# Performance work log

Measured on AMD Instinct MI355X. Metric: run time of the kernel, lower is better.

The kernel has to match this reference:

```python
import jax, jax.numpy as jnp
import numpy as np
from jax.scipy.linalg import solve_triangular

OMEGA0 = 30.0  # standard SIREN first-layer frequency


def setup_inputs() -> dict:
    key = jax.random.key(0)
    ks = jax.random.split(key, 12)
    B, NC, NT, XD, H, R = 64, 1024, 1024, 1, 512, 512
    x_context = jax.random.normal(ks[0], (B, NC, XD), jnp.float32)
    y_context = jax.random.normal(ks[1], (B, NC, 1), jnp.float32)
    x_target = jax.random.normal(ks[2], (B, NT, XD), jnp.float32)
    # SIREN MLP params (hidden_dims=[512,512,512], repr_dim=512)
    def lin(k, fi, fo, first=False):
        bound = 1.0 / fi if first else np.sqrt(6.0 / fi) / OMEGA0
        kW, kb = jax.random.split(k)
        W = jax.random.uniform(kW, (fi, fo), jnp.float32, -bound, bound)
        b = jax.random.uniform(kb, (fo,), jnp.float32, -bound, bound)
        return W, b
    W0, b0 = lin(ks[3], XD, H, first=True)
    W1, b1 = lin(ks[4], H, H)
    W2, b2 = lin(ks[5], H, H)
    Wr, br = lin(ks[6], H, R)
    log_noise_var = jnp.asarray(np.log(0.01), jnp.float32)
    return {"x_context": x_context, "y_context": y_context, "x_target": x_target,
            "W0": W0, "b0": b0, "W1": W1, "b1": b1, "W2": W2, "b2": b2,
            "Wr": Wr, "br": br, "log_noise_var": log_noise_var}


def _mlp(x, W0, b0, W1, b1, W2, b2, Wr, br):
    # SIREN: sine activations, omega_0 on first layer, linear head
    h = jnp.sin(OMEGA0 * (x @ W0 + b0))
    h = jnp.sin(h @ W1 + b1)
    h = jnp.sin(h @ W2 + b2)
    return h @ Wr + br


def reference(x_context, y_context, x_target, W0, b0, W1, b1, W2, b2, Wr, br, log_noise_var):
    mean = jnp.mean(y_context, axis=1, keepdims=True)          # [B,1,1]
    std = jnp.std(y_context, axis=1, keepdims=True, ddof=1)    # torch.std is unbiased
    yc = (y_context - mean) / std                              # [B,N,1]

    cr = _mlp(x_context, W0, b0, W1, b1, W2, b2, Wr, br)       # [B,N,R]
    tr = _mlp(x_target, W0, b0, W1, b1, W2, b2, Wr, br)        # [B,M,R]
    ones_c = jnp.ones(cr.shape[:-1] + (1,), cr.dtype)
    ones_t = jnp.ones(tr.shape[:-1] + (1,), tr.dtype)
    cr = jnp.concatenate([cr, ones_c], axis=-1)                # [B,N,R+1]
    tr = jnp.concatenate([tr, ones_t], axis=-1)                # [B,M,R+1]

    Rp1 = cr.shape[-1]
    cov = jnp.einsum('bnr,bns->brs', cr, cr)                   # [B,R+1,R+1]
    cov = cov + jnp.exp(log_noise_var) * jnp.eye(Rp1, dtype=cov.dtype)
    xty = jnp.einsum('bnr,bnd->brd', cr, yc)                   # [B,R+1,1]

    chol = jnp.linalg.cholesky(cov)                            # batched potrf
    z = solve_triangular(chol, xty, lower=True)
    w = solve_triangular(jnp.swapaxes(chol, -1, -2), z, lower=False)  # [B,R+1,1]

    y_pred = tr @ w                                            # [B,M,1]
    return y_pred * std + mean
```

## Files before the change

### kernel.cpp

```cpp
#include <hip/hip_runtime.h>
#include <hip/hip_fp16.h>
#include <math.h>

#define NB    64
#define NPTS  1024
#define HD    512
#define CPAD  576
#define COVE  ((size_t)NB*CPAD*CPAD)

typedef __attribute__((ext_vector_type(4))) float v4f;
typedef __attribute__((ext_vector_type(8))) short v8s;
typedef __attribute__((ext_vector_type(8))) _Float16 v8h;

__device__ __forceinline__ float sin_poly(float z){
  float t = z*z;
  float p = fmaf(t, -1.9841270e-4f, 8.3333333e-3f);
  p = fmaf(t, p, -0.16666667f);
  p = fmaf(t, p, 1.0f);
  return z*p;
}

__device__ __forceinline__ ushort2 split_f16(float a){
  _Float16 h = (_Float16)a;
  float hf = (float)h;
  _Float16 l = (_Float16)(a - hf);
  unsigned short uh, ul;
  __builtin_memcpy(&uh, &h, 2);
  __builtin_memcpy(&ul, &l, 2);
  ushort2 r; r.x = uh; r.y = ul;
  return r;
}

__device__ __forceinline__ unsigned short f16b(float a){
  _Float16 h = (_Float16)a;
  unsigned short uh; __builtin_memcpy(&uh, &h, 2);
  return uh;
}

__device__ __forceinline__ float f16r(float a){
  return (float)(_Float16)a;
}

__device__ __forceinline__ void g2l16(const unsigned short* g, unsigned short* l){
  __builtin_amdgcn_global_load_lds(
      (const __attribute__((address_space(1))) unsigned int*)(g),
      (__attribute__((address_space(3))) unsigned int*)(l), 16, 0, 0);
}

__global__ __launch_bounds__(256)
void prep_k(const float* __restrict__ W1, const float* __restrict__ W2,
            const float* __restrict__ Wr, unsigned short* __restrict__ wf)
{
  __shared__ unsigned short tile[64][65];
  const int mat = blockIdx.x >> 6;
  const int t = blockIdx.x & 63;
  const int k0 = (t >> 3)*64, n0 = (t & 7)*64;
  const float* W = (mat==0) ? W1 : ((mat==1) ? W2 : Wr);
  const int tid = threadIdx.x;
  for (int idx=tid; idx<4096; idx+=256){
    int r = idx >> 6, c = idx & 63;
    tile[r][c] = f16b(W[(size_t)(k0+r)*512 + n0 + c]);
  }
  __syncthreads();
  unsigned short* dst = wf + (size_t)mat*262144;
  for (int idx=tid; idx<4096; idx+=256){
    int r = idx >> 6, c = idx & 63;
    dst[(size_t)(n0+r)*512 + k0 + c] = tile[c][r];
  }
}

__device__ __forceinline__ void h0c(const float* __restrict__ w0,
                                    const float* __restrict__ b0, int K0, int sq,
                                    float xv0, float xv1, v8s& pa0, v8s& pa1)
{
  const float* wp = w0 + K0 + sq*8;
  const float* bp = b0 + K0 + sq*8;
  float4 wva = *(const float4*)wp, wvb = *(const float4*)(wp+4);
  float4 bva = *(const float4*)bp, bvb = *(const float4*)(bp+4);
  float w8[8] = {wva.x,wva.y,wva.z,wva.w,wvb.x,wvb.y,wvb.z,wvb.w};
  float b8[8] = {bva.x,bva.y,bva.z,bva.w,bvb.x,bvb.y,bvb.z,bvb.w};
  #pragma unroll
  for (int i=0;i<8;++i){
    pa0[i] = (short)f16b(__sinf(30.f*fmaf(xv0, w8[i], b8[i])));
    pa1[i] = (short)f16b(__sinf(30.f*fmaf(xv1, w8[i], b8[i])));
  }
}

template<int EPI, int TRANS, int AMODE>
__global__ __launch_bounds__(256, 2)
void gemm_ld(const unsigned short* __restrict__ Ap,
             const float* __restrict__ xsrc, const float* __restrict__ w0,
             const float* __restrict__ b0,
             const unsigned short* __restrict__ Bw,
             const float* __restrict__ bias,
             unsigned short* __restrict__ Chi, unsigned short* __restrict__ Clo,
             const float* __restrict__ vvp, float* __restrict__ ydot, int rowBase)
{
  __shared__ unsigned short Ah[2][4096], Bh[2][8192];
  const int tid  = threadIdx.x;
  const int lane = tid & 63, wave = tid >> 6;
  const int wm = wave & 1, wn = wave >> 1;
  const int m0 = blockIdx.x*128, n0 = blockIdx.y*256;
  const int q = lane >> 4, ln16 = lane & 15;
  const int sr = tid >> 2, sq = tid & 3;
  const int qx  = (q ^ ((ln16>>1)&3))*8;
  const int swc = ((lane&3) ^ ((lane>>3)&3))*8;
  const int wsl = (sq ^ ((sr>>1)&3))*8;

  const int strowA = wave*32 + (lane>>2);
  const int strowB = wave*64 + (lane>>2);
  const unsigned short* gA = Ap + (size_t)(m0 + strowA)*512 + swc;
  const unsigned short* gB = Bw + (size_t)(n0 + strowB)*512 + swc;

  float xv0 = 0.f, xv1 = 0.f;
  if (AMODE == 1){ xv0 = xsrc[m0 + sr]; xv1 = xsrc[m0 + sr + 64]; }

  v4f acc[4][8];
  #pragma unroll
  for (int a=0;a<4;++a)
    #pragma unroll
    for (int b=0;b<8;++b) acc[a][b] = (v4f)(0.0f);

  v8s pa0, pa1;
  if (AMODE == 0){
    g2l16(gA, Ah[0]+wave*1024); g2l16(gA+16*512, Ah[0]+wave*1024+512);
  } else {
    h0c(w0, b0, 0, sq, xv0, xv1, pa0, pa1);
    *(v8s*)(Ah[0] + sr*32 + wsl) = pa0;
    *(v8s*)(Ah[0] + (sr+64)*32 + wsl) = pa1;
  }
  #pragma unroll
  for (int m=0;m<4;++m) g2l16(gB + m*16*512, Bh[0]+wave*2048 + m*512);
  __syncthreads();

  int cur = 0;
  for (int ks=0; ks<16; ++ks){
    const int nxt = cur^1;
    if (ks < 15){
      const int k1 = (ks+1)*32;
      if (AMODE == 0){
        g2l16(gA+k1, Ah[nxt]+wave*1024); g2l16(gA+k1+16*512, Ah[nxt]+wave*1024+512);
      }
      #pragma unroll
      for (int m=0;m<4;++m) g2l16(gB + k1 + m*16*512, Bh[nxt]+wave*2048 + m*512);
    }
    v8h bhf[8];
    #pragma unroll
    for (int nt=0; nt<8; ++nt){
      const int nrow = wn*128 + nt*16 + ln16;
      bhf[nt] = *(const v8h*)(Bh[cur] + nrow*32 + qx);
    }
    #pragma unroll
    for (int mt=0; mt<4; ++mt){
      const int mrow = wm*64 + mt*16 + ln16;
      v8h ah = *(const v8h*)(Ah[cur] + mrow*32 + qx);
      #pragma unroll
      for (int nt=0; nt<8; ++nt)
        acc[mt][nt] = __builtin_amdgcn_mfma_f32_16x16x32_f16(ah, bhf[nt], acc[mt][nt], 0,0,0);
    }
    if (AMODE == 1 && ks < 15){
      h0c(w0, b0, (ks+1)*32, sq, xv0, xv1, pa0, pa1);
      *(v8s*)(Ah[nxt] + sr*32 + wsl) = pa0;
      *(v8s*)(Ah[nxt] + (sr+64)*32 + wsl) = pa1;
    }
    __syncthreads();
    cur = nxt;
  }

  if (TRANS == 0){
    #pragma unroll
    for (int nt=0;nt<8;++nt){
      const int col = n0 + wn*128 + nt*16 + ln16;
      const float bl_ = bias[col];
      #pragma unroll
      for (int mt=0;mt<4;++mt){
        const int row0 = m0 + wm*64 + mt*16 + q*4;
        #pragma unroll
        for (int r=0;r<4;++r){
          float v = acc[mt][nt][r] + bl_;
          if (EPI == 1) v = sin_poly(v);
          Chi[(size_t)(row0+r)*512 + col] = f16b(v);
        }
      }
    }
  } else if (TRANS == 1){
    const int lb = m0 >> 10;
    #pragma unroll
    for (int nt=0;nt<8;++nt){
      const int col = n0 + wn*128 + nt*16 + ln16;
      const float bl_ = bias[col];
      #pragma unroll
      for (int mt=0;mt<4;++mt){
        const int row0 = m0 + wm*64 + mt*16 + q*4;
        const int nb = row0 & 1023;
        ushort4 h,l; ushort2 s;
        s=split_f16(acc[mt][nt][0]+bl_); h.x=s.x; l.x=s.y;
        s=split_f16(acc[mt][nt][1]+bl_); h.y=s.x; l.y=s.y;
        s=split_f16(acc[mt][nt][2]+bl_); h.z=s.x; l.z=s.y;
        s=split_f16(acc[mt][nt][3]+bl_); h.w=s.x; l.w=s.y;
        size_t o = ((size_t)lb*512 + col)*1024 + nb;
        *(ushort4*)(Chi + o) = h;
        *(ushort4*)(Clo + o) = l;
      }
    }
  } else {
    const int b = (rowBase + m0) >> 10;
    const float* vb = vvp + (size_t)b*512;
    float vcol[8];
    float bl_[8];
    #pragma unroll
    for (int nt=0;nt<8;++nt){
      const int col = n0 + wn*128 + nt*16 + ln16;
      vcol[nt] = vb[col];
      bl_[nt] = bias[col];
    }
    #pragma unroll
    for (int mt=0;mt<4;++mt){
      #pragma unroll
      for (int r=0;r<4;++r){
        float part = 0.f;
        #pragma unroll
        for (int nt=0;nt<8;++nt)
          part = fmaf(sin_poly(acc[mt][nt][r] + bl_[nt]), vcol[nt], part);
        #pragma unroll
        for (int off=1; off<16; off<<=1) part += __shfl_xor(part, off, 64);
        if (ln16 == 0){
          const int row = m0 + wm*64 + mt*16 + q*4 + r;
          atomicAdd(&ydot[rowBase + row], part);
        }
      }
    }
  }
}

__device__ __forceinline__ void ld_ext_row(const unsigned short* __restrict__ h,
                                           const unsigned short* __restrict__ l,
                                           const float* __restrict__ ycn,
                                           int f, int nofs, v8s& oh, v8s& ol)
{
  if (f < 512){
    oh = *(const v8s*)(h + (size_t)f*1024 + nofs);
    ol = *(const v8s*)(l + (size_t)f*1024 + nofs);
  } else if (f == 512){
    #pragma unroll
    for (int j=0;j<8;++j){ oh[j] = (short)0x3C00; ol[j] = 0; }
  } else if (f == 513){
    #pragma unroll
    for (int j=0;j<8;++j){
      ushort2 s = split_f16(ycn[nofs+j]);
      oh[j] = (short)s.x; ol[j] = (short)s.y;
    }
  } else {
    #pragma unroll
    for (int j=0;j<8;++j){ oh[j] = 0; ol[j] = 0; }
  }
}

__global__ __launch_bounds__(256)
void cov_ld(const unsigned short* __restrict__ CThi, const unsigned short* __restrict__ CTlo,
            const float* __restrict__ ycb,
            const float* __restrict__ lnv, float* __restrict__ cov, int bStart)
{
  int t = blockIdx.y;
  int ti = 0;
  while ((ti+1)*(ti+2)/2 <= t) ++ti;
  int tj = t - ti*(ti+1)/2;
  const int i0 = ti*128, j0 = tj*128;
  const int lb = blockIdx.x;
  const int b  = bStart + lb;
  const unsigned short* srch = CThi + (size_t)lb*512*1024;
  const unsigned short* srcl = CTlo + (size_t)lb*512*1024;
  const float* ycn = ycb + (size_t)b*NPTS;
  float* covb = cov + (size_t)b*CPAD*CPAD;
  const float noise = expf(lnv[0]);
  const bool diag = (i0 == j0);
  const bool aReg = (i0 == 512);

  __shared__ unsigned short Ah[2][4096], Al[2][4096], Bh2[2][4096], Bl2[2][4096];
  const int tid = threadIdx.x;
  const int lane = tid & 63, wave = tid >> 6;
  const int wm = wave & 1, wn = wave >> 1;
  const int q = lane >> 4, ln16 = lane & 15;
  const int sr = tid >> 2, sq = tid & 3;
  const int qx  = (q ^ ((ln16>>1)&3))*8;
  const int swc = ((lane&3) ^ ((lane>>3)&3))*8;
  const int wsl = (sq ^ ((sr>>1)&3))*8;

  const int strow = wave*32 + (lane>>2);
  const size_t gaOff = (size_t)(i0 + strow)*1024 + swc;
  const size_t gbOff = (size_t)(j0 + strow)*1024 + swc;
  const int wb = wave*1024;

  v4f acc[4][4];
  #pragma unroll
  for (int a=0;a<4;++a)
    #pragma unroll
    for (int c=0;c<4;++c) acc[a][c] = (v4f)(0.0f);

  if (!aReg){
    g2l16(srch + gaOff, Ah[0]+wb); g2l16(srch + gaOff + (size_t)16*1024, Ah[0]+wb+512);
    g2l16(srcl + gaOff, Al[0]+wb); g2l16(srcl + gaOff + (size_t)16*1024, Al[0]+wb+512);
  } else {
    v8s th, tl;
    ld_ext_row(srch, srcl, ycn, i0 + sr, sq*8, th, tl);
    *(v8s*)(Ah[0] + sr*32 + wsl) = th; *(v8s*)(Al[0] + sr*32 + wsl) = tl;
    ld_ext_row(srch, srcl, ycn, i0 + sr + 64, sq*8, th, tl);
    *(v8s*)(Ah[0] + (sr+64)*32 + wsl) = th; *(v8s*)(Al[0] + (sr+64)*32 + wsl) = tl;
  }
  if (!diag){
    g2l16(srch + gbOff, Bh2[0]+wb); g2l16(srch + gbOff + (size_t)16*1024, Bh2[0]+wb+512);
    g2l16(srcl + gbOff, Bl2[0]+wb); g2l16(srcl + gbOff + (size_t)16*1024, Bl2[0]+wb+512);
  }
  __syncthreads();

  int cur = 0;
  for (int ks=0; ks<32; ++ks){
    const int nxt = cur^1;
    if (ks < 31){
      const int k1 = (ks+1)*32;
      if (!aReg){
        g2l16(srch + gaOff + k1, Ah[nxt]+wb);
        g2l16(srch + gaOff + k1 + (size_t)16*1024, Ah[nxt]+wb+512);
        g2l16(srcl + gaOff + k1, Al[nxt]+wb);
        g2l16(srcl + gaOff + k1 + (size_t)16*1024, Al[nxt]+wb+512);
      }
      if (!diag){
        g2l16(srch + gbOff + k1, Bh2[nxt]+wb);
        g2l16(srch + gbOff + k1 + (size_t)16*1024, Bh2[nxt]+wb+512);
        g2l16(srcl + gbOff + k1, Bl2[nxt]+wb);
        g2l16(srcl + gbOff + k1 + (size_t)16*1024, Bl2[nxt]+wb+512);
      }
    }
    const unsigned short* BhP = diag ? Ah[cur] : Bh2[cur];
    const unsigned short* BlP = diag ? Al[cur] : Bl2[cur];
    v8h bhf[4], blf[4];
    #pragma unroll
    for (int nt=0; nt<4; ++nt){
      const int nrow = wn*64 + nt*16 + ln16;
      bhf[nt] = *(const v8h*)(BhP + nrow*32 + qx);
      blf[nt] = *(const v8h*)(BlP + nrow*32 + qx);
    }
    #pragma unroll
    for (int mt=0; mt<4; ++mt){
      const int mrow = wm*64 + mt*16 + ln16;
      v8h ah = *(const v8h*)(Ah[cur] + mrow*32 + qx);
      v8h al = *(const v8h*)(Al[cur] + mrow*32 + qx);
      #pragma unroll
      for (int nt=0; nt<4; ++nt){
        acc[mt][nt] = __builtin_amdgcn_mfma_f32_16x16x32_f16(ah, bhf[nt], acc[mt][nt], 0,0,0);
        acc[mt][nt] = __builtin_amdgcn_mfma_f32_16x16x32_f16(ah, blf[nt], acc[mt][nt], 0,0,0);
        acc[mt][nt] = __builtin_amdgcn_mfma_f32_16x16x32_f16(al, bhf[nt], acc[mt][nt], 0,0,0);
      }
    }
    if (aReg && ks < 31){
      const int n1 = (ks+1)*32 + sq*8;
      v8s th, tl;
      ld_ext_row(srch, srcl, ycn, i0 + sr, n1, th, tl);
      *(v8s*)(Ah[nxt] + sr*32 + wsl) = th; *(v8s*)(Al[nxt] + sr*32 + wsl) = tl;
      ld_ext_row(srch, srcl, ycn, i0 + sr + 64, n1, th, tl);
      *(v8s*)(Ah[nxt] + (sr+64)*32 + wsl) = th; *(v8s*)(Al[nxt] + (sr+64)*32 + wsl) = tl;
    }
    __syncthreads();
    cur = nxt;
  }
  #pragma unroll
  for (int nt=0;nt<4;++nt){
    const int gj = j0 + wn*64 + nt*16 + ln16;
    #pragma unroll
    for (int mt=0;mt<4;++mt){
      const int gi0 = i0 + wm*64 + mt*16 + q*4;
      #pragma unroll
      for (int r=0;r<4;++r){
        const int gi = gi0 + r;
        if (gj <= gi && gi < CPAD && gj < CPAD){
          float v = acc[mt][nt][r];
          if (gi == gj) v += (gi < 513) ? noise : 1.0f;
          covb[(size_t)gi*CPAD + gj] = v;
        }
      }
    }
  }
}

__global__ __launch_bounds__(256)
void chol_trsm_k(float* __restrict__ cov, float* __restrict__ dchol, int k)
{
  (void)dchol;
  float* Ab = cov + (size_t)blockIdx.x * CPAD * CPAD;
  const int o = k*64;
  const int row0 = o + 64 + blockIdx.y*128;
  const int nrows = min(128, CPAD - row0);
  __shared__ float Ds[64][65];
  __shared__ float As[128][65];
  __shared__ float invd[64];
  const int tid = threadIdx.x;

  for (int idx=tid; idx<nrows*16; idx+=256){
    int r = idx >> 4, c = (idx & 15)*4;
    float4 v = *(const float4*)(Ab + (size_t)(row0+r)*CPAD + o + c);
    As[r][c]=v.x; As[r][c+1]=v.y; As[r][c+2]=v.z; As[r][c+3]=v.w;
  }

  if (tid < 64){
    float a[64];
    const float* rowp = Ab + (size_t)(o+tid)*CPAD + o;
    #pragma unroll
    for (int c=0; c<64; c+=4){
      float4 v = *(const float4*)(rowp + c);
      a[c]   = (c   <= tid) ? v.x : 0.f;
      a[c+1] = (c+1 <= tid) ? v.y : 0.f;
      a[c+2] = (c+2 <= tid) ? v.z : 0.f;
      a[c+3] = (c+3 <= tid) ? v.w : 0.f;
    }
    #pragma unroll
    for (int j=0; j<63; ++j){
      float vj = a[j];
      float t = vj * (1.0f / __shfl(vj, j, 64));
      #pragma unroll
      for (int c=j+1; c<64; ++c)
        a[c] = fmaf(-t, __shfl(vj, c, 64), a[c]);
    }
    float myinv = 0.f;
    #pragma unroll
    for (int c=0; c<64; ++c){
      float ic = 1.0f / sqrtf(__shfl(a[c], c, 64));
      a[c] *= ic;
      myinv = (c == tid) ? ic : myinv;
    }
    invd[tid] = myinv;
    #pragma unroll
    for (int c=0; c<64; ++c) Ds[tid][c] = a[c];
  }
  __syncthreads();

  const int srow = tid - 64;
  if (srow >= 0 && srow < nrows){
    float x[64];
    #pragma unroll
    for (int c=0; c<64; ++c){
      float s0 = As[srow][c], s1 = 0.f, s2 = 0.f, s3 = 0.f;
      #pragma unroll
      for (int j=0; j+4<=c; j+=4){
        s0 = fmaf(-x[j],   Ds[c][j],   s0);
        s1 = fmaf(-x[j+1], Ds[c][j+1], s1);
        s2 = fmaf(-x[j+2], Ds[c][j+2], s2);
        s3 = fmaf(-x[j+3], Ds[c][j+3], s3);
      }
      #pragma unroll
      for (int j = c & ~3; j < c; ++j)
        s0 = fmaf(-x[j], Ds[c][j], s0);
      x[c] = ((s0+s1)+(s2+s3)) * invd[c];
    }
    #pragma unroll
    for (int c=0; c<64; ++c) As[srow][c] = x[c];
  } else if (blockIdx.y == 0 && tid >= 192){
    const int r = tid - 192;
    float y[64];
    #pragma unroll
    for (int c = 63; c >= 0; --c){
      float s0 = (c == r) ? 1.0f : 0.0f, s1 = 0.f, s2 = 0.f, s3 = 0.f;
      #pragma unroll
      for (int j = c+1; j+4 <= 64; j += 4){
        s0 = fmaf(-Ds[j][c],   y[j],   s0);
        s1 = fmaf(-Ds[j+1][c], y[j+1], s1);
        s2 = fmaf(-Ds[j+2][c], y[j+2], s2);
        s3 = fmaf(-Ds[j+3][c], y[j+3], s3);
      }
      #pragma unroll
      for (int j = c+1 + ((63-c) & ~3); j < 64; ++j)
        s0 = fmaf(-Ds[j][c], y[j], s0);
      y[c] = ((s0+s1)+(s2+s3)) * invd[c];
    }
    float* dst = Ab + (size_t)(o + r)*CPAD + 512;
    #pragma unroll
    for (int c = 0; c < 64; c += 4)
      *(float4*)(dst + c) = make_float4(y[c], y[c+1], y[c+2], y[c+3]);
  }
  __syncthreads();
  for (int idx=tid; idx<nrows*16; idx+=256){
    int r = idx >> 4, c = (idx & 15)*4;
    float4 v = make_float4(As[r][c], As[r][c+1], As[r][c+2], As[r][c+3]);
    *(float4*)(Ab + (size_t)(row0+r)*CPAD + o + c) = v;
  }
}

__global__ __launch_bounds__(256)
void chol_trail_k(float* __restrict__ cov, int k)
{
  float* Ab = cov + (size_t)blockIdx.y * CPAD * CPAD;
  int t = blockIdx.x;
  int bi = 0;
  while ((bi+1)*(bi+2)/2 <= t) ++bi;
  int bj = t - bi*(bi+1)/2;
  const int o = k*64;
  const int s0 = o + 64;
  const int I = s0 + bi*64, J = s0 + bj*64;
  const bool diag = (bi == bj);

  __shared__ unsigned short Pih[64*72], Pil[64*72], Pjh[64*72], Pjl[64*72];
  const int tid = threadIdx.x;
  const int lane = tid & 63, wave = tid >> 6;
  const int q = lane >> 4, ln16 = lane & 15;

  for (int idx=tid; idx<1024; idx+=256){
    int r = idx >> 4, c = (idx & 15)*4;
    float4 v = *(const float4*)(Ab + (size_t)(I+r)*CPAD + o + c);
    ushort4 hh, ll; ushort2 s;
    s=split_f16(v.x); hh.x=s.x; ll.x=s.y;
    s=split_f16(v.y); hh.y=s.x; ll.y=s.y;
    s=split_f16(v.z); hh.z=s.x; ll.z=s.y;
    s=split_f16(v.w); hh.w=s.x; ll.w=s.y;
    *(ushort4*)(Pih + r*72 + c) = hh;
    *(ushort4*)(Pil + r*72 + c) = ll;
    if (!diag){
      float4 u = *(const float4*)(Ab + (size_t)(J+r)*CPAD + o + c);
      s=split_f16(u.x); hh.x=s.x; ll.x=s.y;
      s=split_f16(u.y); hh.y=s.x; ll.y=s.y;
      s=split_f16(u.z); hh.z=s.x; ll.z=s.y;
      s=split_f16(u.w); hh.w=s.x; ll.w=s.y;
      *(ushort4*)(Pjh + r*72 + c) = hh;
      *(ushort4*)(Pjl + r*72 + c) = ll;
    }
  }
  __syncthreads();
  const unsigned short* Bh = diag ? Pih : Pjh;
  const unsigned short* Bl = diag ? Pil : Pjl;

  v4f acc[4];
  #pragma unroll
  for (int nt=0;nt<4;++nt) acc[nt] = (v4f)(0.0f);

  #pragma unroll
  for (int ks=0; ks<2; ++ks){
    const int ko = ks*32 + q*8;
    v8h ah = *(const v8h*)(Pih + (wave*16 + ln16)*72 + ko);
    v8h al = *(const v8h*)(Pil + (wave*16 + ln16)*72 + ko);
    #pragma unroll
    for (int nt=0; nt<4; ++nt){
      v8h bh = *(const v8h*)(Bh + (nt*16 + ln16)*72 + ko);
      v8h bl = *(const v8h*)(Bl + (nt*16 + ln16)*72 + ko);
      acc[nt] = __builtin_amdgcn_mfma_f32_16x16x32_f16(ah, bh, acc[nt], 0,0,0);
      acc[nt] = __builtin_amdgcn_mfma_f32_16x16x32_f16(ah, bl, acc[nt], 0,0,0);
      acc[nt] = __builtin_amdgcn_mfma_f32_16x16x32_f16(al, bh, acc[nt], 0,0,0);
    }
  }

  #pragma unroll
  for (int nt=0; nt<4; ++nt){
    const int gj = J + nt*16 + ln16;
    #pragma unroll
    for (int r=0; r<4; ++r){
      const int gi = I + wave*16 + q*4 + r;
      if (gj <= gi)
        Ab[(size_t)gi*CPAD + gj] -= acc[nt][r];
    }
  }
}

__global__ __launch_bounds__(256)
void chol_last_k(float* __restrict__ cov, float* __restrict__ dchol)
{
  float* Ab = cov + (size_t)blockIdx.x * CPAD * CPAD;
  __shared__ float P[64][65];
  __shared__ float Ds[64][65];
  __shared__ float invl[64];
  const int tid = threadIdx.x;

  for (int idx=tid; idx<1024; idx+=256){
    int r = idx >> 4, c = (idx & 15)*4;
    float4 v = *(const float4*)(Ab + (size_t)(512+r)*CPAD + 448 + c);
    P[r][c]=v.x; P[r][c+1]=v.y; P[r][c+2]=v.z; P[r][c+3]=v.w;
    float4 u = *(const float4*)(Ab + (size_t)(512+r)*CPAD + 512 + c);
    Ds[r][c]   = (c   <= r) ? u.x : 0.f;
    Ds[r][c+1] = (c+1 <= r) ? u.y : 0.f;
    Ds[r][c+2] = (c+2 <= r) ? u.z : 0.f;
    Ds[r][c+3] = (c+3 <= r) ? u.w : 0.f;
  }
  __syncthreads();
  {
    const int tx = tid & 15, ty = tid >> 4;
    float acc[4][4];
    #pragma unroll
    for (int r=0;r<4;++r)
      #pragma unroll
      for (int c=0;c<4;++c) acc[r][c]=0.f;
    for (int kk=0; kk<64; ++kk){
      float av[4], bv[4];
      #pragma unroll
      for (int r=0;r<4;++r) av[r] = P[tx*4+r][kk];
      #pragma unroll
      for (int c=0;c<4;++c) bv[c] = P[ty*4+c][kk];
      #pragma unroll
      for (int r=0;r<4;++r)
        #pragma unroll
        for (int c=0;c<4;++c) acc[r][c] = fmaf(av[r], bv[c], acc[r][c]);
    }
    __syncthreads();
    #pragma unroll
    for (int r=0;r<4;++r){
      int gi = tx*4 + r;
      #pragma unroll
      for (int c=0;c<4;++c){
        int gj = ty*4 + c;
        if (gj <= gi) Ds[gi][gj] -= acc[r][c];
      }
    }
  }
  __syncthreads();

  if (tid < 64){
    float a[64];
    #pragma unroll
    for (int c=0; c<64; ++c) a[c] = Ds[tid][c];
    #pragma unroll
    for (int j=0; j<63; ++j){
      float vj = a[j];
      float t = vj * (1.0f / __shfl(vj, j, 64));
      #pragma unroll
      for (int c=j+1; c<64; ++c)
        a[c] = fmaf(-t, __shfl(vj, c, 64), a[c]);
    }
    float myinv = 0.f;
    #pragma unroll
    for (int c=0; c<64; ++c){
      float ic = 1.0f / sqrtf(__shfl(a[c], c, 64));
      a[c] *= ic;
      myinv = (c == tid) ? ic : myinv;
    }
    invl[tid] = myinv;
    #pragma unroll
    for (int c=0; c<64; ++c) Ds[tid][c] = a[c];
  }
  __syncthreads();

  float* dst = dchol + ((size_t)blockIdx.x*9 + 8)*4096;
  for (int idx=tid; idx<4096; idx+=256)
    dst[idx] = Ds[idx>>6][idx&63];
  if (tid < 64){
    const int r = tid;
    float y[64];
    #pragma unroll
    for (int c = 63; c >= 0; --c){
      float s0 = (c == r) ? 1.0f : 0.0f, s1 = 0.f, s2 = 0.f, s3 = 0.f;
      #pragma unroll
      for (int j = c+1; j+4 <= 64; j += 4){
        s0 = fmaf(-Ds[j][c],   y[j],   s0);
        s1 = fmaf(-Ds[j+1][c], y[j+1], s1);
        s2 = fmaf(-Ds[j+2][c], y[j+2], s2);
        s3 = fmaf(-Ds[j+3][c], y[j+3], s3);
      }
      #pragma unroll
      for (int j = c+1 + ((63-c) & ~3); j < 64; ++j)
        s0 = fmaf(-Ds[j][c], y[j], s0);
      y[c] = ((s0+s1)+(s2+s3)) * invl[c];
    }
    float* dst2 = Ab + (size_t)(512 + r)*CPAD + 512;
    #pragma unroll
    for (int c = 0; c < 64; c += 4)
      *(float4*)(dst2 + c) = make_float4(y[c], y[c+1], y[c+2], y[c+3]);
  }
}

__global__ __launch_bounds__(1024)
void back_solve_k(const float* __restrict__ cov, const float* __restrict__ dchol,
                  float* __restrict__ wv)
{
  const int b = blockIdx.x;
  const float* L = cov + (size_t)b*CPAD*CPAD;
  const float* dc = dchol + (size_t)b*9*4096;
  __shared__ float inv2[64*64];
  __shared__ float rhs[CPAD];
  __shared__ float xv[64];
  __shared__ float red[4*512];
  const int tid = threadIdx.x;
  const int pr = tid >> 4, pc = (tid & 15)*4;
  const float* zrow = L + (size_t)513*CPAD;

  for (int i=tid; i<CPAD; i+=1024)
    rhs[i] = (i < 512) ? zrow[i] : ((i == 512) ? dc[8*4096 + 64] : 0.f);
  {
    float4 v = *(const float4*)(L + (size_t)(512 + pr)*CPAD + 512 + pc);
    *(float4*)(inv2 + pr*64 + pc) = v;
  }
  __syncthreads();

  for (int k=8; k>=1; --k){
    const int o = k*64;
    const int G = o >> 2;
    const int act = G << 2;
    float4 v16[16];
    int rg = 0, cg = 0;
    if (tid < act){
      rg = tid / G; cg = tid % G;
      const float* lp = L + (size_t)(o + rg*16)*CPAD + cg*4;
      #pragma unroll
      for (int rr=0; rr<16; ++rr)
        v16[rr] = *(const float4*)(lp + (size_t)rr*CPAD);
    }
    float4 pf = *(const float4*)(L + (size_t)((k-1)*64 + pr)*CPAD + 512 + pc);
    if (tid < 64){
      float acc = 0.f;
      #pragma unroll
      for (int j=0;j<64;++j) acc = fmaf(inv2[j*64 + tid], rhs[o+j], acc);
      xv[tid] = acc;
      rhs[o+tid] = acc;
    }
    __syncthreads();
    if (tid < act){
      float4 s = {0.f,0.f,0.f,0.f};
      #pragma unroll
      for (int rr=0; rr<16; ++rr){
        float xr = xv[rg*16 + rr];
        s.x = fmaf(v16[rr].x, xr, s.x);
        s.y = fmaf(v16[rr].y, xr, s.y);
        s.z = fmaf(v16[rr].z, xr, s.z);
        s.w = fmaf(v16[rr].w, xr, s.w);
      }
      *(float4*)(red + rg*512 + cg*4) = s;
    }
    __syncthreads();
    if (tid < o)
      rhs[tid] -= (red[tid] + red[512+tid]) + (red[1024+tid] + red[1536+tid]);
    *(float4*)(inv2 + pr*64 + pc) = pf;
    __syncthreads();
  }
  if (tid < 64){
    float acc = 0.f;
    #pragma unroll
    for (int j=0;j<64;++j) acc = fmaf(inv2[j*64 + tid], rhs[j], acc);
    rhs[tid] = acc;
  }
  __syncthreads();
  for (int i=tid; i<CPAD; i+=1024) wv[(size_t)b*CPAD + i] = rhs[i];
}

__global__ __launch_bounds__(512)
void fold_k(const float* __restrict__ Wr, const float* __restrict__ br,
            const float* __restrict__ wv, float* __restrict__ vv, float* __restrict__ cvec)
{
  int b = blockIdx.x, j = threadIdx.x;
  const float* wb = wv + (size_t)b*CPAD;
  __shared__ float ws_[512];
  __shared__ float red[512];
  ws_[j] = wb[j];
  __syncthreads();
  float acc = 0.f;
  const float* row = Wr + (size_t)j*512;
  for (int r=0; r<512; r+=4){
    float4 w4 = *(const float4*)(row + r);
    acc = fmaf(f16r(w4.x), ws_[r],   acc);
    acc = fmaf(f16r(w4.y), ws_[r+1], acc);
    acc = fmaf(f16r(w4.z), ws_[r+2], acc);
    acc = fmaf(f16r(w4.w), ws_[r+3], acc);
  }
  vv[(size_t)b*512 + j] = acc;
  red[j] = br[j]*ws_[j];
  __syncthreads();
  for (int s=256; s>0; s>>=1){ if (j<s) red[j]+=red[j+s]; __syncthreads(); }
  if (j == 0) cvec[b] = red[0] + wb[512];
}

__global__ __launch_bounds__(256)
void stats_k(const float* __restrict__ y, float* __restrict__ meanv,
             float* __restrict__ stdv, float* __restrict__ ycb)
{
  int b = blockIdx.x, tid = threadIdx.x;
  const float* yb = y + (size_t)b*NPTS;
  float4 v = *(const float4*)(yb + tid*4);
  float s  = v.x+v.y+v.z+v.w;
  float ss = v.x*v.x+v.y*v.y+v.z*v.z+v.w*v.w;
  #pragma unroll
  for (int off=32; off; off>>=1){ s += __shfl_down(s, off); ss += __shfl_down(ss, off); }
  __shared__ float rs[4], rss[4], bc[2];
  int wid = tid>>6, lane = tid&63;
  if (lane == 0){ rs[wid]=s; rss[wid]=ss; }
  __syncthreads();
  if (tid == 0){
    float S  = rs[0]+rs[1]+rs[2]+rs[3];
    float SS = rss[0]+rss[1]+rss[2]+rss[3];
    float mean = S * (1.0f/NPTS);
    float var  = (SS - S*S*(1.0f/NPTS)) * (1.0f/(NPTS-1));
    float sd = sqrtf(var);
    meanv[b]=mean; stdv[b]=sd; bc[0]=mean; bc[1]=1.0f/sd;
  }
  __syncthreads();
  float mean=bc[0], inv=bc[1];
  float4 o;
  o.x=(v.x-mean)*inv; o.y=(v.y-mean)*inv; o.z=(v.z-mean)*inv; o.w=(v.w-mean)*inv;
  *(float4*)(ycb + (size_t)b*NPTS + tid*4) = o;
}

__global__ __launch_bounds__(256)
void fin_k(const float* __restrict__ ydot, const float* __restrict__ cvec,
           const float* __restrict__ meanv, const float* __restrict__ stdv,
           float* __restrict__ out)
{
  int i = blockIdx.x*256 + threadIdx.x;
  int b = i >> 10;
  out[i] = fmaf(ydot[i] + cvec[b], stdv[b], meanv[b]);
}

extern "C" void kernel_launch(void* const* d_in, const int* in_sizes, int n_in,
                              void* d_out, int out_size, void* d_ws, size_t ws_size,
                              hipStream_t stream)
{
  (void)in_sizes; (void)n_in; (void)out_size;
  const float* x_ctx = (const float*)d_in[0];
  const float* y_ctx = (const float*)d_in[1];
  const float* x_tgt = (const float*)d_in[2];
  const float* W0 = (const float*)d_in[3];
  const float* b0 = (const float*)d_in[4];
  const float* W1 = (const float*)d_in[5];
  const float* b1 = (const float*)d_in[6];
  const float* W2 = (const float*)d_in[7];
  const float* b2 = (const float*)d_in[8];
  const float* Wr = (const float*)d_in[9];
  const float* br = (const float*)d_in[10];
  const float* lnv = (const float*)d_in[11];
  float* out = (float*)d_out;
  float* ws = (float*)d_ws;

  int CH = 65536;
  for (;;){
    size_t fl = COVE + 65536 + 192 + (size_t)64*512 + (size_t)64*CPAD + 65536
              + (size_t)64*9*4096 + 64;
    size_t sh = (size_t)3*262144 + (size_t)2*CH*512 + (size_t)2*(CH/1024)*512*1024;
    size_t need = fl*4 + sh*2;
    if (ws_size >= need || CH <= 1024) break;
    CH >>= 1;
  }
  const int nch = 65536 / CH;
  const int bpc = CH / NPTS;

  float* cov   = ws;
  float* ycb   = cov + COVE;
  float* meanv = ycb + 65536;
  float* stdv  = meanv + 64;
  float* cvec  = stdv + 64;
  float* vvb   = cvec + 64;
  float* wvb   = vvb + (size_t)64*512;
  float* ydot  = wvb + (size_t)64*CPAD;
  float* dchol = ydot + 65536;
  unsigned short* wf   = (unsigned short*)(dchol + (size_t)64*9*4096);
  unsigned short* P0   = wf + (size_t)3*262144;
  unsigned short* P1   = P0 + (size_t)CH*512;
  unsigned short* CThi = P1 + (size_t)CH*512;
  unsigned short* CTlo = CThi + (size_t)bpc*512*1024;

  prep_k<<<192, 256, 0, stream>>>(W1, W2, Wr, wf);
  stats_k<<<NB, 256, 0, stream>>>(y_ctx, meanv, stdv, ycb);

  for (int c=0; c<nch; ++c){
    const float* xc = x_ctx + (size_t)c*CH;
    dim3 g(CH/128, 2);
    gemm_ld<1,0,1><<<g, 256, 0, stream>>>(0, xc, W0, b0, wf, b1, P1, 0, 0, 0, 0);
    gemm_ld<1,0,0><<<g, 256, 0, stream>>>(P1, 0, 0, 0, wf+262144, b2, P0, 0, 0, 0, 0);
    gemm_ld<0,1,0><<<g, 256, 0, stream>>>(P0, 0, 0, 0, wf+524288, br, CThi, CTlo, 0, 0, 0);
    cov_ld<<<dim3(bpc, 15), 256, 0, stream>>>(CThi, CTlo, ycb, lnv, cov, c*bpc);
  }

  for (int k=0; k<8; ++k){
    const int cnt = CPAD - k*64 - 64;
    chol_trsm_k<<<dim3(NB, (cnt + 127)/128), 256, 0, stream>>>(cov, dchol, k);
    if (k < 7){
      const int tcnt = cnt >> 6;
      chol_trail_k<<<dim3(tcnt*(tcnt+1)/2, NB), 256, 0, stream>>>(cov, k);
    }
  }
  chol_last_k<<<NB, 256, 0, stream>>>(cov, dchol);
  back_solve_k<<<NB, 1024, 0, stream>>>(cov, dchol, wvb);
  fold_k<<<NB, 512, 0, stream>>>(Wr, br, wvb, vvb, cvec);

  hipMemsetAsync(ydot, 0, 65536*sizeof(float), stream);
  for (int c=0; c<nch; ++c){
    const float* xt = x_tgt + (size_t)c*CH;
    dim3 g(CH/128, 2);
    gemm_ld<1,0,1><<<g, 256, 0, stream>>>(0, xt, W0, b0, wf, b1, P1, 0, 0, 0, 0);
    gemm_ld<1,2,0><<<g, 256, 0, stream>>>(P1, 0, 0, 0, wf+262144, b2, 0, 0, vvb, ydot, c*CH);
  }
  fin_k<<<256, 256, 0, stream>>>(ydot, cvec, meanv, stdv, out);
}
```

Baseline: 1.086 ms.

## Fuse last three Cholesky panels into one kernel and merge small launches

Replaces the final two trsm/trail iterations and chol_last with one per-batch kernel that factors the trailing 192x192 block in shared memory. It also folds fold_k and the ydot memset into back_solve_k, and stats_k into prep_k. A third change skips one redundant wave's MFMA work in diagonal cov tiles. The aim is to cut kernel launches and per-launch overhead in the sequential tail, at the cost of a large shared-memory footprint and serial per-block work with low occupancy.

After: 1.246 ms. +14.8%, slower.

```diff
diff --git a/kernel.cpp b/kernel.cpp
--- a/kernel.cpp
+++ b/kernel.cpp
@@ -49,14 +49,43 @@
 
 __global__ __launch_bounds__(256)
 void prep_k(const float* __restrict__ W1, const float* __restrict__ W2,
-            const float* __restrict__ Wr, unsigned short* __restrict__ wf)
+            const float* __restrict__ Wr, unsigned short* __restrict__ wf,
+            const float* __restrict__ y, float* __restrict__ meanv,
+            float* __restrict__ stdv, float* __restrict__ ycb)
 {
   __shared__ unsigned short tile[64][65];
+  __shared__ float rs[4], rss[4], bc[2];
+  const int tid = threadIdx.x;
+  if (blockIdx.x >= 192){
+    const int b = blockIdx.x - 192;
+    const float* yb = y + (size_t)b*NPTS;
+    float4 v = *(const float4*)(yb + tid*4);
+    float s  = v.x+v.y+v.z+v.w;
+    float ss = v.x*v.x+v.y*v.y+v.z*v.z+v.w*v.w;
+    #pragma unroll
+    for (int off=32; off; off>>=1){ s += __shfl_down(s, off); ss += __shfl_down(ss, off); }
+    int wid = tid>>6, lane = tid&63;
+    if (lane == 0){ rs[wid]=s; rss[wid]=ss; }
+    __syncthreads();
+    if (tid == 0){
+      float S  = rs[0]+rs[1]+rs[2]+rs[3];
+      float SS = rss[0]+rss[1]+rss[2]+rss[3];
+      float mean = S * (1.0f/NPTS);
+      float var  = (SS - S*S*(1.0f/NPTS)) * (1.0f/(NPTS-1));
+      float sd = sqrtf(var);
+      meanv[b]=mean; stdv[b]=sd; bc[0]=mean; bc[1]=1.0f/sd;
+    }
+    __syncthreads();
+    float mean=bc[0], inv=bc[1];
+    float4 o;
+    o.x=(v.x-mean)*inv; o.y=(v.y-mean)*inv; o.z=(v.z-mean)*inv; o.w=(v.w-mean)*inv;
+    *(float4*)(ycb + (size_t)b*NPTS + tid*4) = o;
+    return;
+  }
   const int mat = blockIdx.x >> 6;
   const int t = blockIdx.x & 63;
   const int k0 = (t >> 3)*64, n0 = (t & 7)*64;
   const float* W = (mat==0) ? W1 : ((mat==1) ? W2 : Wr);
-  const int tid = threadIdx.x;
   for (int idx=tid; idx<4096; idx+=256){
     int r = idx >> 6, c = idx & 63;
     tile[r][c] = f16b(W[(size_t)(k0+r)*512 + n0 + c]);
@@ -285,6 +314,7 @@
   const int qx  = (q ^ ((ln16>>1)&3))*8;
   const int swc = ((lane&3) ^ ((lane>>3)&3))*8;
   const int wsl = (sq ^ ((sr>>1)&3))*8;
+  const bool skipW = diag && (wave == 2);
 
   const int strow = wave*32 + (lane>>2);
   const size_t gaOff = (size_t)(i0 + strow)*1024 + swc;
@@ -331,25 +361,27 @@
         g2l16(srcl + gbOff + k1 + (size_t)16*1024, Bl2[nxt]+wb+512);
       }
     }
-    const unsigned short* BhP = diag ? Ah[cur] : Bh2[cur];
-    const unsigned short* BlP = diag ? Al[cur] : Bl2[cur];
-    v8h bhf[4], blf[4];
-    #pragma unroll
-    for (int nt=0; nt<4; ++nt){
-      const int nrow = wn*64 + nt*16 + ln16;
-      bhf[nt] = *(const v8h*)(BhP + nrow*32 + qx);
-      blf[nt] = *(const v8h*)(BlP + nrow*32 + qx);
-    }
-    #pragma unroll
-    for (int mt=0; mt<4; ++mt){
-      const int mrow = wm*64 + mt*16 + ln16;
-      v8h ah = *(const v8h*)(Ah[cur] + mrow*32 + qx);
-      v8h al = *(const v8h*)(Al[cur] + mrow*32 + qx);
+    if (!skipW){
+      const unsigned short* BhP = diag ? Ah[cur] : Bh2[cur];
+      const unsigned short* BlP = diag ? Al[cur] : Bl2[cur];
+      v8h bhf[4], blf[4];
       #pragma unroll
       for (int nt=0; nt<4; ++nt){
-        acc[mt][nt] = __builtin_amdgcn_mfma_f32_16x16x32_f16(ah, bhf[nt], acc[mt][nt], 0,0,0);
-        acc[mt][nt] = __builtin_amdgcn_mfma_f32_16x16x32_f16(ah, blf[nt], acc[mt][nt], 0,0,0);
-        acc[mt][nt] = __builtin_amdgcn_mfma_f32_16x16x32_f16(al, bhf[nt], acc[mt][nt], 0,0,0);
+        const int nrow = wn*64 + nt*16 + ln16;
+        bhf[nt] = *(const v8h*)(BhP + nrow*32 + qx);
+        blf[nt] = *(const v8h*)(BlP + nrow*32 + qx);
+      }
+      #pragma unroll
+      for (int mt=0; mt<4; ++mt){
+        const int mrow = wm*64 + mt*16 + ln16;
+        v8h ah = *(const v8h*)(Ah[cur] + mrow*32 + qx);
+        v8h al = *(const v8h*)(Al[cur] + mrow*32 + qx);
+        #pragma unroll
+        for (int nt=0; nt<4; ++nt){
+          acc[mt][nt] = __builtin_amdgcn_mfma_f32_16x16x32_f16(ah, bhf[nt], acc[mt][nt], 0,0,0);
+          acc[mt][nt] = __builtin_amdgcn_mfma_f32_16x16x32_f16(ah, blf[nt], acc[mt][nt], 0,0,0);
+          acc[mt][nt] = __builtin_amdgcn_mfma_f32_16x16x32_f16(al, bhf[nt], acc[mt][nt], 0,0,0);
+        }
       }
     }
     if (aReg && ks < 31){
@@ -558,112 +590,138 @@
 }
 
 __global__ __launch_bounds__(256)
-void chol_last_k(float* __restrict__ cov, float* __restrict__ dchol)
+void chol_tail_k(float* __restrict__ cov, float* __restrict__ dchol)
 {
   float* Ab = cov + (size_t)blockIdx.x * CPAD * CPAD;
-  __shared__ float P[64][65];
-  __shared__ float Ds[64][65];
-  __shared__ float invl[64];
+  __shared__ float T[192][196];
+  __shared__ float invd3[3][64];
   const int tid = threadIdx.x;
 
-  for (int idx=tid; idx<1024; idx+=256){
-    int r = idx >> 4, c = (idx & 15)*4;
-    float4 v = *(const float4*)(Ab + (size_t)(512+r)*CPAD + 448 + c);
-    P[r][c]=v.x; P[r][c+1]=v.y; P[r][c+2]=v.z; P[r][c+3]=v.w;
-    float4 u = *(const float4*)(Ab + (size_t)(512+r)*CPAD + 512 + c);
-    Ds[r][c]   = (c   <= r) ? u.x : 0.f;
-    Ds[r][c+1] = (c+1 <= r) ? u.y : 0.f;
-    Ds[r][c+2] = (c+2 <= r) ? u.z : 0.f;
-    Ds[r][c+3] = (c+3 <= r) ? u.w : 0.f;
-  }
-  __syncthreads();
-  {
-    const int tx = tid & 15, ty = tid >> 4;
-    float acc[4][4];
-    #pragma unroll
-    for (int r=0;r<4;++r)
-      #pragma unroll
-      for (int c=0;c<4;++c) acc[r][c]=0.f;
-    for (int kk=0; kk<64; ++kk){
-      float av[4], bv[4];
-      #pragma unroll
-      for (int r=0;r<4;++r) av[r] = P[tx*4+r][kk];
-      #pragma unroll
-      for (int c=0;c<4;++c) bv[c] = P[ty*4+c][kk];
-      #pragma unroll
-      for (int r=0;r<4;++r)
+  for (int idx=tid; idx<192*48; idx+=256){
+    int r = idx/48, c4 = (idx%48)*4;
+    float4 v = *(const float4*)(Ab + (size_t)(384+r)*CPAD + 384 + c4);
+    T[r][c4]=v.x; T[r][c4+1]=v.y; T[r][c4+2]=v.z; T[r][c4+3]=v.w;
+  }
+  __syncthreads();
+
+  #pragma unroll
+  for (int s=0; s<3; ++s){
+    const int ob = s*64;
+    const int nr = 128 - ob;
+    if (tid < 64){
+      float a[64];
+      #pragma unroll
+      for (int c=0;c<64;++c) a[c] = (c <= tid) ? T[ob+tid][ob+c] : 0.f;
+      #pragma unroll
+      for (int j=0;j<63;++j){
+        float vj = a[j];
+        float tt = vj * (1.0f/__shfl(vj, j, 64));
         #pragma unroll
-        for (int c=0;c<4;++c) acc[r][c] = fmaf(av[r], bv[c], acc[r][c]);
+        for (int c=j+1;c<64;++c)
+          a[c] = fmaf(-tt, __shfl(vj, c, 64), a[c]);
+      }
+      float myinv = 0.f;
+      #pragma unroll
+      for (int c=0;c<64;++c){
+        float ic = 1.0f/sqrtf(__shfl(a[c], c, 64));
+        a[c] *= ic;
+        myinv = (c==tid) ? ic : myinv;
+      }
+      invd3[s][tid] = myinv;
+      #pragma unroll
+      for (int c=0;c<64;++c) T[ob+tid][ob+c] = a[c];
     }
     __syncthreads();
-    #pragma unroll
-    for (int r=0;r<4;++r){
-      int gi = tx*4 + r;
-      #pragma unroll
-      for (int c=0;c<4;++c){
-        int gj = ty*4 + c;
-        if (gj <= gi) Ds[gi][gj] -= acc[r][c];
-      }
-    }
-  }
-  __syncthreads();
-
-  if (tid < 64){
-    float a[64];
-    #pragma unroll
-    for (int c=0; c<64; ++c) a[c] = Ds[tid][c];
-    #pragma unroll
-    for (int j=0; j<63; ++j){
-      float vj = a[j];
-      float t = vj * (1.0f / __shfl(vj, j, 64));
-      #pragma unroll
-      for (int c=j+1; c<64; ++c)
-        a[c] = fmaf(-t, __shfl(vj, c, 64), a[c]);
-    }
-    float myinv = 0.f;
-    #pragma unroll
-    for (int c=0; c<64; ++c){
-      float ic = 1.0f / sqrtf(__shfl(a[c], c, 64));
-      a[c] *= ic;
-      myinv = (c == tid) ? ic : myinv;
-    }
-    invl[tid] = myinv;
-    #pragma unroll
-    for (int c=0; c<64; ++c) Ds[tid][c] = a[c];
-  }
-  __syncthreads();
-
-  float* dst = dchol + ((size_t)blockIdx.x*9 + 8)*4096;
+    if (nr > 0){
+      if (tid < nr){
+        const int ri = ob + 64 + tid;
+        float x[64];
+        #pragma unroll
+        for (int c=0;c<64;++c){
+          float s0 = T[ri][ob+c], s1=0.f, s2=0.f, s3=0.f;
+          #pragma unroll
+          for (int j=0;j+4<=c;j+=4){
+            s0 = fmaf(-x[j],   T[ob+c][ob+j],   s0);
+            s1 = fmaf(-x[j+1], T[ob+c][ob+j+1], s1);
+            s2 = fmaf(-x[j+2], T[ob+c][ob+j+2], s2);
+            s3 = fmaf(-x[j+3], T[ob+c][ob+j+3], s3);
+          }
+          #pragma unroll
+          for (int j=c&~3;j<c;++j) s0 = fmaf(-x[j], T[ob+c][ob+j], s0);
+          x[c] = ((s0+s1)+(s2+s3)) * invd3[s][c];
+        }
+        #pragma unroll
+        for (int c=0;c<64;++c) T[ri][ob+c] = x[c];
+      }
+      __syncthreads();
+      {
+        const int row = tid & 127, half = tid >> 7;
+        if (row < nr){
+          const int gi = ob + 64 + row;
+          for (int j=half; j<=row; j+=2){
+            const int gj = ob + 64 + j;
+            float s0=0.f,s1=0.f,s2=0.f,s3=0.f;
+            #pragma unroll
+            for (int c=0;c<64;c+=4){
+              s0 = fmaf(T[gi][ob+c],   T[gj][ob+c],   s0);
+              s1 = fmaf(T[gi][ob+c+1], T[gj][ob+c+1], s1);
+              s2 = fmaf(T[gi][ob+c+2], T[gj][ob+c+2], s2);
+              s3 = fmaf(T[gi][ob+c+3], T[gj][ob+c+3], s3);
+            }
+            T[gi][gj] -= (s0+s1)+(s2+s3);
+          }
+        }
+      }
+      __syncthreads();
+    }
+  }
+
+  if (tid < 192){
+    const int s = tid >> 6, r = tid & 63, ob = s*64;
+    float y[64];
+    #pragma unroll
+    for (int c=63;c>=0;--c){
+      float s0 = (c==r)?1.f:0.f, s1=0.f,s2=0.f,s3=0.f;
+      #pragma unroll
+      for (int j=c+1;j+4<=64;j+=4){
+        s0 = fmaf(-T[ob+j][ob+c],   y[j],   s0);
+        s1 = fmaf(-T[ob+j+1][ob+c], y[j+1], s1);
+        s2 = fmaf(-T[ob+j+2][ob+c], y[j+2], s2);
+        s3 = fmaf(-T[ob+j+3][ob+c], y[j+3], s3);
+      }
+      #pragma unroll
+      for (int j=c+1+((63-c)&~3); j<64; ++j)
+        s0 = fmaf(-T[ob+j][ob+c], y[j], s0);
+      y[c] = ((s0+s1)+(s2+s3)) * invd3[s][c];
+    }
+    float* dst = Ab + (size_t)(384 + ob + r)*CPAD + 512;
+    #pragma unroll
+    for (int c=0;c<64;c+=4)
+      *(float4*)(dst + c) = make_float4(y[c], y[c+1], y[c+2], y[c+3]);
+  }
+
+  float* dst8 = dchol + ((size_t)blockIdx.x*9 + 8)*4096;
   for (int idx=tid; idx<4096; idx+=256)
-    dst[idx] = Ds[idx>>6][idx&63];
-  if (tid < 64){
-    const int r = tid;
-    float y[64];
-    #pragma unroll
-    for (int c = 63; c >= 0; --c){
-      float s0 = (c == r) ? 1.0f : 0.0f, s1 = 0.f, s2 = 0.f, s3 = 0.f;
-      #pragma unroll
-      for (int j = c+1; j+4 <= 64; j += 4){
-        s0 = fmaf(-Ds[j][c],   y[j],   s0);
-        s1 = fmaf(-Ds[j+1][c], y[j+1], s1);
-        s2 = fmaf(-Ds[j+2][c], y[j+2], s2);
-        s3 = fmaf(-Ds[j+3][c], y[j+3], s3);
-      }
-      #pragma unroll
-      for (int j = c+1 + ((63-c) & ~3); j < 64; ++j)
-        s0 = fmaf(-Ds[j][c], y[j], s0);
-      y[c] = ((s0+s1)+(s2+s3)) * invl[c];
-    }
-    float* dst2 = Ab + (size_t)(512 + r)*CPAD + 512;
-    #pragma unroll
-    for (int c = 0; c < 64; c += 4)
-      *(float4*)(dst2 + c) = make_float4(y[c], y[c+1], y[c+2], y[c+3]);
+    dst8[idx] = T[128 + (idx>>6)][128 + (idx&63)];
+
+  for (int idx=tid; idx<192*48; idx+=256){
+    int r = idx/48, c4 = (idx%48)*4;
+    const int gr = 384 + r;
+    float* rp = Ab + (size_t)gr*CPAD;
+    #pragma unroll
+    for (int e=0;e<4;++e){
+      const int gc = 384 + c4 + e;
+      if (gc <= gr && !(gr >= 512 && gc >= 512))
+        rp[gc] = T[r][c4+e];
+    }
   }
 }
 
 __global__ __launch_bounds__(1024)
 void back_solve_k(const float* __restrict__ cov, const float* __restrict__ dchol,
-                  float* __restrict__ wv)
+                  const float* __restrict__ Wr, const float* __restrict__ br,
+                  float* __restrict__ vv, float* __restrict__ cvec,
+                  float* __restrict__ ydot)
 {
   const int b = blockIdx.x;
   const float* L = cov + (size_t)b*CPAD*CPAD;
@@ -731,63 +789,32 @@
     rhs[tid] = acc;
   }
   __syncthreads();
-  for (int i=tid; i<CPAD; i+=1024) wv[(size_t)b*CPAD + i] = rhs[i];
-}
-
-__global__ __launch_bounds__(512)
-void fold_k(const float* __restrict__ Wr, const float* __restrict__ br,
-            const float* __restrict__ wv, float* __restrict__ vv, float* __restrict__ cvec)
-{
-  int b = blockIdx.x, j = threadIdx.x;
-  const float* wb = wv + (size_t)b*CPAD;
-  __shared__ float ws_[512];
-  __shared__ float red[512];
-  ws_[j] = wb[j];
-  __syncthreads();
-  float acc = 0.f;
-  const float* row = Wr + (size_t)j*512;
-  for (int r=0; r<512; r+=4){
-    float4 w4 = *(const float4*)(row + r);
-    acc = fmaf(f16r(w4.x), ws_[r],   acc);
-    acc = fmaf(f16r(w4.y), ws_[r+1], acc);
-    acc = fmaf(f16r(w4.z), ws_[r+2], acc);
-    acc = fmaf(f16r(w4.w), ws_[r+3], acc);
-  }
-  vv[(size_t)b*512 + j] = acc;
-  red[j] = br[j]*ws_[j];
-  __syncthreads();
-  for (int s=256; s>0; s>>=1){ if (j<s) red[j]+=red[j+s]; __syncthreads(); }
-  if (j == 0) cvec[b] = red[0] + wb[512];
-}
-
-__global__ __launch_bounds__(256)
-void stats_k(const float* __restrict__ y, float* __restrict__ meanv,
-             float* __restrict__ stdv, float* __restrict__ ycb)
-{
-  int b = blockIdx.x, tid = threadIdx.x;
-  const float* yb = y + (size_t)b*NPTS;
-  float4 v = *(const float4*)(yb + tid*4);
-  float s  = v.x+v.y+v.z+v.w;
-  float ss = v.x*v.x+v.y*v.y+v.z*v.z+v.w*v.w;
-  #pragma unroll
-  for (int off=32; off; off>>=1){ s += __shfl_down(s, off); ss += __shfl_down(ss, off); }
-  __shared__ float rs[4], rss[4], bc[2];
-  int wid = tid>>6, lane = tid&63;
-  if (lane == 0){ rs[wid]=s; rss[wid]=ss; }
-  __syncthreads();
-  if (tid == 0){
-    float S  = rs[0]+rs[1]+rs[2]+rs[3];
-    float SS = rss[0]+rss[1]+rss[2]+rss[3];
-    float mean = S * (1.0f/NPTS);
-    float var  = (SS - S*S*(1.0f/NPTS)) * (1.0f/(NPTS-1));
-    float sd = sqrtf(var);
-    meanv[b]=mean; stdv[b]=sd; bc[0]=mean; bc[1]=1.0f/sd;
-  }
-  __syncthreads();
-  float mean=bc[0], inv=bc[1];
-  float4 o;
-  o.x=(v.x-mean)*inv; o.y=(v.y-mean)*inv; o.z=(v.z-mean)*inv; o.w=(v.w-mean)*inv;
-  *(float4*)(ycb + (size_t)b*NPTS + tid*4) = o;
+
+  ydot[(size_t)b*1024 + tid] = 0.f;
+  const int j = tid >> 1, h = tid & 1;
+  {
+    float acc = 0.f;
+    const float* row = Wr + (size_t)j*512 + h*256;
+    const float* wsp = rhs + h*256;
+    for (int r=0; r<256; r+=4){
+      float4 w4 = *(const float4*)(row + r);
+      acc = fmaf(f16r(w4.x), wsp[r],   acc);
+      acc = fmaf(f16r(w4.y), wsp[r+1], acc);
+      acc = fmaf(f16r(w4.z), wsp[r+2], acc);
+      acc = fmaf(f16r(w4.w), wsp[r+3], acc);
+    }
+    red[tid] = acc;
+  }
+  __syncthreads();
+  if (h == 0) vv[(size_t)b*512 + j] = red[tid] + red[tid+1];
+  __syncthreads();
+  red[tid] = (tid < 512) ? br[tid]*rhs[tid] : 0.f;
+  __syncthreads();
+  for (int s2=512; s2>0; s2>>=1){
+    if (tid < s2) red[tid] += red[tid+s2];
+    __syncthreads();
+  }
+  if (tid == 0) cvec[b] = red[0] + rhs[512];
 }
 
 __global__ __launch_bounds__(256)
@@ -847,8 +874,7 @@
   unsigned short* CThi = P1 + (size_t)CH*512;
   unsigned short* CTlo = CThi + (size_t)bpc*512*1024;
 
-  prep_k<<<192, 256, 0, stream>>>(W1, W2, Wr, wf);
-  stats_k<<<NB, 256, 0, stream>>>(y_ctx, meanv, stdv, ycb);
+  prep_k<<<256, 256, 0, stream>>>(W1, W2, Wr, wf, y_ctx, meanv, stdv, ycb);
 
   for (int c=0; c<nch; ++c){
     const float* xc = x_ctx + (size_t)c*CH;
@@ -859,19 +885,15 @@
     cov_ld<<<dim3(bpc, 15), 256, 0, stream>>>(CThi, CTlo, ycb, lnv, cov, c*bpc);
   }
 
-  for (int k=0; k<8; ++k){
+  for (int k=0; k<6; ++k){
     const int cnt = CPAD - k*64 - 64;
     chol_trsm_k<<<dim3(NB, (cnt + 127)/128), 256, 0, stream>>>(cov, dchol, k);
-    if (k < 7){
-      const int tcnt = cnt >> 6;
-      chol_trail_k<<<dim3(tcnt*(tcnt+1)/2, NB), 256, 0, stream>>>(cov, k);
-    }
-  }
-  chol_last_k<<<NB, 256, 0, stream>>>(cov, dchol);
-  back_solve_k<<<NB, 1024, 0, stream>>>(cov, dchol, wvb);
-  fold_k<<<NB, 512, 0, stream>>>(Wr, br, wvb, vvb, cvec);
-
-  hipMemsetAsync(ydot, 0, 65536*sizeof(float), stream);
+    const int tcnt = cnt >> 6;
+    chol_trail_k<<<dim3(tcnt*(tcnt+1)/2, NB), 256, 0, stream>>>(cov, k);
+  }
+  chol_tail_k<<<NB, 256, 0, stream>>>(cov, dchol);
+  back_solve_k<<<NB, 1024, 0, stream>>>(cov, dchol, Wr, br, vvb, cvec, ydot);
+
   for (int c=0; c<nch; ++c){
     const float* xt = x_tgt + (size_t)c*CH;
     dim3 g(CH/128, 2);
```
